# Kernel tuning notes

Hardware: AMD Instinct MI355X
Metric: run time of the kernel (lower is better)

Reference implementation:

```python
import jax, jax.numpy as jnp
import numpy as np

NEG_BIG = -9e15  # matches torch's -9000000000000000.0 masked-fill value
ALPHA = 0.2      # LeakyReLU negative slope


def setup_inputs() -> dict:
    key = jax.random.key(0)
    k1, k2, k3, k4 = jax.random.split(key, 4)
    N, F_in, F_out = 8192, 128, 64
    h = jax.random.normal(k1, (N, F_in), dtype=jnp.float32)
    adj = jax.random.randint(k2, (N, N), 0, 2).astype(jnp.float32)
    # Glorot(gain=1.414)-scale params
    W = jax.random.normal(k3, (F_in, F_out), dtype=jnp.float32) * (1.414 * np.sqrt(2.0 / (F_in + F_out)))
    a = jax.random.normal(k4, (2 * F_out, 1), dtype=jnp.float32) * (1.414 * np.sqrt(2.0 / (2 * F_out + 1)))
    return {"h": h, "adj": adj, "W": W, "a": a}


def reference(h, adj, W, a):
    F_out = W.shape[1]
    Wh = h @ W                               # [N, F_out]
    Wh1 = Wh @ a[:F_out, :]                  # [N, 1]
    Wh2 = Wh @ a[F_out:, :]                  # [N, 1]
    e = jax.nn.leaky_relu(Wh1 + Wh2.T, negative_slope=ALPHA)  # [N, N]
    attention = jnp.where(adj > 0, e, NEG_BIG)
    attention = jax.nn.softmax(attention, axis=1)
    # dropout omitted (eval mode / p applied only in training)
    h_prime = attention @ Wh                 # [N, F_out]
    return jax.nn.elu(h_prime)               # concat=True -> ELU
```

## Files before the change

kernel.cpp:

```cpp
#include <hip/hip_runtime.h>
#include <hip/hip_bf16.h>

#define N 8192
#define FIN 128
#define FOUT 64
#define ALPHA 0.2f
#define LOG2E 1.44269504f
#define JSPLIT 4
#define JSPAN (N / JSPLIT)
#define STJ 128
#define NST (JSPAN / STJ)

typedef __attribute__((ext_vector_type(8))) short short8;
typedef __attribute__((ext_vector_type(4))) float f32x4;

static __device__ __forceinline__ unsigned fkey(float x) {
    unsigned u = __float_as_uint(x);
    return (u >> 31) ? ~u : (u | 0x80000000u);
}
static __device__ __forceinline__ float fdecode(unsigned k) {
    unsigned u = (k & 0x80000000u) ? (k & 0x7FFFFFFFu) : ~k;
    return __uint_as_float(u);
}
static __device__ __forceinline__ void gll16(const float* g, float* l) {
    __builtin_amdgcn_global_load_lds(
        (const __attribute__((address_space(1))) unsigned int*)g,
        (__attribute__((address_space(3))) unsigned int*)l, 16, 0, 0);
}

__global__ __launch_bounds__(256) void k_prep(const float* __restrict__ h,
                                              const float* __restrict__ W,
                                              const float* __restrict__ a,
                                              float* __restrict__ Wh,
                                              float* __restrict__ s2,
                                              float* __restrict__ t2,
                                              unsigned* __restrict__ keys) {
    __shared__ float lH[16 * FIN];
    __shared__ float lW[FIN * FOUT];
    __shared__ float red[8];
    const int tid = threadIdx.x;
    const int r0 = blockIdx.x * 16;
    {
        const float4* src = (const float4*)(h + (size_t)r0 * FIN);
        float4* dst = (float4*)lH;
        for (int i = tid; i < 16 * FIN / 4; i += 256) dst[i] = src[i];
        const float4* ws_ = (const float4*)W;
        float4* dw = (float4*)lW;
        for (int i = tid; i < FIN * FOUT / 4; i += 256) dw[i] = ws_[i];
    }
    __syncthreads();
    const int wave = tid >> 6, lane = tid & 63;
    float acc[4] = {0.f, 0.f, 0.f, 0.f};
    for (int k = 0; k < FIN; ++k) {
        float wv = lW[k * FOUT + lane];
#pragma unroll
        for (int r = 0; r < 4; ++r)
            acc[r] = fmaf(lH[(wave * 4 + r) * FIN + k], wv, acc[r]);
    }
    const float a1 = a[lane], a2 = a[FOUT + lane];
    float smx = -1e30f, tmx = -1e30f;
#pragma unroll
    for (int r = 0; r < 4; ++r) {
        int row = r0 + wave * 4 + r;
        Wh[(size_t)row * FOUT + lane] = acc[r];
        float sv = acc[r] * a1, tv = acc[r] * a2;
#pragma unroll
        for (int off = 32; off; off >>= 1) {
            sv += __shfl_xor(sv, off);
            tv += __shfl_xor(tv, off);
        }
        sv *= LOG2E; tv *= LOG2E;
        if (lane == 0) { s2[row] = sv; t2[row] = tv; }
        smx = fmaxf(smx, sv);
        tmx = fmaxf(tmx, tv);
    }
    if (lane == 0) { red[wave] = smx; red[4 + wave] = tmx; }
    __syncthreads();
    if (tid == 0) {
        float ms = fmaxf(fmaxf(red[0], red[1]), fmaxf(red[2], red[3]));
        float mt = fmaxf(fmaxf(red[4], red[5]), fmaxf(red[6], red[7]));
        atomicMax(keys + 0, fkey(ms));
        atomicMax(keys + 1, fkey(mt));
    }
}

__global__ __launch_bounds__(256) void k_pack(const float* __restrict__ Wh,
                                              __hip_bfloat16* __restrict__ WhB) {
    const int c = blockIdx.x;
    const int tn = threadIdx.x >> 6;
    const int lane = threadIdx.x & 63;
    const int quad = lane >> 4, l16 = lane & 15;
    const float* src = Wh + ((size_t)(c * 32 + quad * 8)) * FOUT + tn * 16 + l16;
    union { unsigned short u[8]; short8 v; } frag;
#pragma unroll
    for (int e = 0; e < 8; ++e) {
        __hip_bfloat16 b = __float2bfloat16(src[(size_t)e * FOUT]);
        frag.u[e] = *(unsigned short*)&b;
    }
    *(short8*)&WhB[(((size_t)c * 4 + tn) * 64 + lane) * 8] = frag.v;
}

__global__ __launch_bounds__(256) void k_attn(const float* __restrict__ adj,
                                              const __hip_bfloat16* __restrict__ WhB,
                                              const float* __restrict__ s2,
                                              const float* __restrict__ t2,
                                              const unsigned* __restrict__ keys,
                                              float* __restrict__ acc_ws,
                                              float* __restrict__ l_ws) {
    __shared__ float smem[2 * 4 * 512];
    __shared__ float smT[2][256];
    __shared__ float shl[4][16];
    const int wave = threadIdx.x >> 6, lane = threadIdx.x & 63;
    const int quad = lane >> 4, l16 = lane & 15;
    const int i0 = blockIdx.x * 16;
    const int jbase = blockIdx.y * JSPAN;

    const float mraw = fdecode(keys[0]) + fdecode(keys[1]);
    const float mm = mraw > 0.f ? mraw : ALPHA * mraw;
    const float sm = s2[i0 + l16];
    const short8* BF = (const short8*)WhB;

    const float* ga = adj + (size_t)(i0 + l16) * N + jbase + wave * 32 + quad * 8;
    const float* gt = t2 + jbase + lane * 4;

    f32x4 acc0 = {0,0,0,0}, acc1 = {0,0,0,0}, acc2 = {0,0,0,0}, acc3 = {0,0,0,0};
    float lsum = 0.f;

    gll16(ga, smem + wave * 512);
    gll16(ga + 4, smem + wave * 512 + 256);
    if (wave == 0) gll16(gt, smT[0]);
    __syncthreads();

    for (int st = 0; st < NST; ++st) {
        const int b = st & 1;
        if (st + 1 < NST) {
            const float* g = ga + (size_t)(st + 1) * STJ;
            float* lb = smem + (b ^ 1) * 2048 + wave * 512;
            gll16(g, lb);
            gll16(g + 4, lb + 256);
            if (wave == 0) gll16(gt + (size_t)(st + 1) * STJ, smT[b ^ 1]);
        }
        const int kc = blockIdx.y * (JSPAN / 32) + st * 4 + wave;
        short8 Bf0 = BF[((size_t)kc * 4 + 0) * 64 + lane];
        short8 Bf1 = BF[((size_t)kc * 4 + 1) * 64 + lane];
        short8 Bf2 = BF[((size_t)kc * 4 + 2) * 64 + lane];
        short8 Bf3 = BF[((size_t)kc * 4 + 3) * 64 + lane];
        const float* Au = smem + b * 2048 + wave * 512;
        float4 alo = *(const float4*)(Au + (lane << 2));
        float4 ahi = *(const float4*)(Au + 256 + (lane << 2));
        const float* Tu = smT[b] + wave * 32 + quad * 8;
        float4 tlo = *(const float4*)(Tu);
        float4 thi = *(const float4*)(Tu + 4);

        union { __hip_bfloat162 h2[4]; short8 v; } af;
#pragma unroll
        for (int pp = 0; pp < 4; ++pp) {
            float a0 = (pp < 2) ? ((const float*)&alo)[2 * pp]     : ((const float*)&ahi)[2 * pp - 4];
            float a1 = (pp < 2) ? ((const float*)&alo)[2 * pp + 1] : ((const float*)&ahi)[2 * pp - 3];
            float t0 = (pp < 2) ? ((const float*)&tlo)[2 * pp]     : ((const float*)&thi)[2 * pp - 4];
            float t1 = (pp < 2) ? ((const float*)&tlo)[2 * pp + 1] : ((const float*)&thi)[2 * pp - 3];
            float x0 = sm + t0,            x1 = sm + t1;
            float le0 = fmaxf(x0, ALPHA * x0), le1 = fmaxf(x1, ALPHA * x1);
            float p0 = a0 * exp2f(le0 - mm),   p1 = a1 * exp2f(le1 - mm);
            __hip_bfloat162 pb = __float22bfloat162_rn(make_float2(p0, p1));
            af.h2[pp] = pb;
            lsum += __bfloat162float(pb.x) + __bfloat162float(pb.y);
        }
        acc0 = __builtin_amdgcn_mfma_f32_16x16x32_bf16(af.v, Bf0, acc0, 0, 0, 0);
        acc1 = __builtin_amdgcn_mfma_f32_16x16x32_bf16(af.v, Bf1, acc1, 0, 0, 0);
        acc2 = __builtin_amdgcn_mfma_f32_16x16x32_bf16(af.v, Bf2, acc2, 0, 0, 0);
        acc3 = __builtin_amdgcn_mfma_f32_16x16x32_bf16(af.v, Bf3, acc3, 0, 0, 0);
        __syncthreads();
    }

    lsum += __shfl_xor(lsum, 16);
    lsum += __shfl_xor(lsum, 32);

    float* accr = smem;
    *(f32x4*)&accr[((wave * 4 + 0) * 64 + lane) * 4] = acc0;
    *(f32x4*)&accr[((wave * 4 + 1) * 64 + lane) * 4] = acc1;
    *(f32x4*)&accr[((wave * 4 + 2) * 64 + lane) * 4] = acc2;
    *(f32x4*)&accr[((wave * 4 + 3) * 64 + lane) * 4] = acc3;
    if (lane < 16) shl[wave][lane] = lsum;
    __syncthreads();

    const int tile = wave;
    f32x4 tot = {0, 0, 0, 0};
#pragma unroll
    for (int w = 0; w < 4; ++w) {
        f32x4 c = *(const f32x4*)&accr[((w * 4 + tile) * 64 + lane) * 4];
        tot[0] += c[0]; tot[1] += c[1]; tot[2] += c[2]; tot[3] += c[3];
    }
#pragma unroll
    for (int r = 0; r < 4; ++r) {
        int row = quad * 4 + r;
        atomicAdd(&acc_ws[(size_t)(i0 + row) * FOUT + tile * 16 + l16], tot[r]);
    }
    if (wave == 0 && lane < 16) {
        float lv = shl[0][lane] + shl[1][lane] + shl[2][lane] + shl[3][lane];
        atomicAdd(&l_ws[i0 + lane], lv);
    }
}

__global__ __launch_bounds__(256) void k_final(const float* __restrict__ acc_ws,
                                               const float* __restrict__ l_ws,
                                               float* __restrict__ out) {
    const int idx = blockIdx.x * 256 + threadIdx.x;
    const int row = idx >> 4;
    const float inv = 1.0f / l_ws[row];
    float4 a = ((const float4*)acc_ws)[idx];
    float4 o;
#pragma unroll
    for (int r = 0; r < 4; ++r) {
        float v = ((const float*)&a)[r] * inv;
        ((float*)&o)[r] = v > 0.f ? v : (exp2f(v * LOG2E) - 1.f);
    }
    ((float4*)out)[idx] = o;
}

extern "C" void kernel_launch(void* const* d_in, const int* in_sizes, int n_in,
                              void* d_out, int out_size, void* d_ws, size_t ws_size,
                              hipStream_t stream) {
    const float* h   = (const float*)d_in[0];
    const float* adj = (const float*)d_in[1];
    const float* W   = (const float*)d_in[2];
    const float* a   = (const float*)d_in[3];
    float* out = (float*)d_out;

    float* Wh = (float*)d_ws;
    __hip_bfloat16* WhB = (__hip_bfloat16*)(Wh + (size_t)N * FOUT);
    float* s2 = (float*)(WhB + (size_t)N * FOUT);
    float* t2 = s2 + N;
    float* pad = t2 + N;
    float* acc_ws = pad + 256;
    float* l_ws = acc_ws + (size_t)N * FOUT;
    unsigned* keys = (unsigned*)(l_ws + N);

    hipMemsetAsync(acc_ws, 0, ((size_t)N * FOUT + N) * sizeof(float) + 2 * sizeof(unsigned),
                   stream);
    k_prep<<<N / 16, 256, 0, stream>>>(h, W, a, Wh, s2, t2, keys);
    k_pack<<<N / 32, 256, 0, stream>>>(Wh, WhB);
    dim3 ag(N / 16, JSPLIT);
    k_attn<<<ag, 256, 0, stream>>>(adj, WhB, s2, t2, keys, acc_ws, l_ws);
    k_final<<<(N * FOUT / 4) / 256, 256, 0, stream>>>(acc_ws, l_ws, out);
}
```

Measured before the change: 415.7 us.

## Split attention into streaming P-matrix kernel and separate MFMA PV kernel

Replaces the fused adjacency-to-MFMA kernel with two passes. The first pass streams adj, computes the masked exp weights, writes them as a bf16 matrix and accumulates row sums. The second pass does a register-prefetched MFMA product into per-split partial buffers, which the final kernel reduces instead of relying on atomics. This trades extra global traffic and a large workspace for simpler, more bandwidth-friendly kernels without LDS sync in the main loop.

```diff
diff --git a/kernel.cpp b/kernel.cpp
--- a/kernel.cpp
+++ b/kernel.cpp
@@ -6,10 +6,9 @@
 #define FOUT 64
 #define ALPHA 0.2f
 #define LOG2E 1.44269504f
-#define JSPLIT 4
-#define JSPAN (N / JSPLIT)
-#define STJ 128
-#define NST (JSPAN / STJ)
+#define KSPLIT 8
+#define KSPAN (N / KSPLIT)
+#define UPW 8
 
 typedef __attribute__((ext_vector_type(8))) short short8;
 typedef __attribute__((ext_vector_type(4))) float f32x4;
@@ -21,11 +20,6 @@
 static __device__ __forceinline__ float fdecode(unsigned k) {
     unsigned u = (k & 0x80000000u) ? (k & 0x7FFFFFFFu) : ~k;
     return __uint_as_float(u);
-}
-static __device__ __forceinline__ void gll16(const float* g, float* l) {
-    __builtin_amdgcn_global_load_lds(
-        (const __attribute__((address_space(1))) unsigned int*)g,
-        (__attribute__((address_space(3))) unsigned int*)l, 16, 0, 0);
 }
 
 __global__ __launch_bounds__(256) void k_prep(const float* __restrict__ h,
@@ -100,105 +94,94 @@
     *(short8*)&WhB[(((size_t)c * 4 + tn) * 64 + lane) * 8] = frag.v;
 }
 
-__global__ __launch_bounds__(256) void k_attn(const float* __restrict__ adj,
-                                              const __hip_bfloat16* __restrict__ WhB,
+__global__ __launch_bounds__(256) void k_pmat(const float* __restrict__ adj,
                                               const float* __restrict__ s2,
                                               const float* __restrict__ t2,
                                               const unsigned* __restrict__ keys,
-                                              float* __restrict__ acc_ws,
+                                              unsigned long long* __restrict__ P,
                                               float* __restrict__ l_ws) {
-    __shared__ float smem[2 * 4 * 512];
-    __shared__ float smT[2][256];
-    __shared__ float shl[4][16];
+    const int tid = blockIdx.x * 256 + threadIdx.x;
+    const int row = tid >> 11;
+    const int j4 = tid & 2047;
+    const int lane = threadIdx.x & 63;
+    const float mraw = fdecode(keys[0]) + fdecode(keys[1]);
+    const float mm = mraw > 0.f ? mraw : ALPHA * mraw;
+    const float sm = s2[row];
+    const float4 av = ((const float4*)adj)[tid];
+    const float4 tv = ((const float4*)t2)[j4];
+    float p[4];
+#pragma unroll
+    for (int e = 0; e < 4; ++e) {
+        float x = sm + ((const float*)&tv)[e];
+        float le = fmaxf(x, ALPHA * x);
+        p[e] = ((const float*)&av)[e] * exp2f(le - mm);
+    }
+    union { __hip_bfloat162 h2[2]; unsigned long long u64; } pk;
+    pk.h2[0] = __float22bfloat162_rn(make_float2(p[0], p[1]));
+    pk.h2[1] = __float22bfloat162_rn(make_float2(p[2], p[3]));
+    P[tid] = pk.u64;
+    float ls = __bfloat162float(pk.h2[0].x) + __bfloat162float(pk.h2[0].y) +
+               __bfloat162float(pk.h2[1].x) + __bfloat162float(pk.h2[1].y);
+#pragma unroll
+    for (int off = 32; off; off >>= 1) ls += __shfl_xor(ls, off);
+    if (lane == 0) atomicAdd(&l_ws[row], ls);
+}
+
+__global__ __launch_bounds__(256) void k_pv(const __hip_bfloat16* __restrict__ P,
+                                            const __hip_bfloat16* __restrict__ WhB,
+                                            float* __restrict__ acc_ws) {
+    __shared__ float ep[4][4][64][4];
     const int wave = threadIdx.x >> 6, lane = threadIdx.x & 63;
     const int quad = lane >> 4, l16 = lane & 15;
     const int i0 = blockIdx.x * 16;
-    const int jbase = blockIdx.y * JSPAN;
-
-    const float mraw = fdecode(keys[0]) + fdecode(keys[1]);
-    const float mm = mraw > 0.f ? mraw : ALPHA * mraw;
-    const float sm = s2[i0 + l16];
+    const int kb = blockIdx.y * KSPAN + wave * 256;
+    const int kc0 = blockIdx.y * (KSPAN / 32) + wave * UPW;
+    const short8* PG = (const short8*)(P + (size_t)(i0 + l16) * N + kb + quad * 8);
     const short8* BF = (const short8*)WhB;
 
-    const float* ga = adj + (size_t)(i0 + l16) * N + jbase + wave * 32 + quad * 8;
-    const float* gt = t2 + jbase + lane * 4;
-
     f32x4 acc0 = {0,0,0,0}, acc1 = {0,0,0,0}, acc2 = {0,0,0,0}, acc3 = {0,0,0,0};
-    float lsum = 0.f;
-
-    gll16(ga, smem + wave * 512);
-    gll16(ga + 4, smem + wave * 512 + 256);
-    if (wave == 0) gll16(gt, smT[0]);
+    short8 Pp[2], B0[2], B1[2], B2[2], B3[2];
+#pragma unroll
+    for (int d = 0; d < 2; ++d) {
+        Pp[d] = PG[d * 4];
+        const size_t c = (size_t)(kc0 + d) * 4;
+        B0[d] = BF[(c + 0) * 64 + lane];
+        B1[d] = BF[(c + 1) * 64 + lane];
+        B2[d] = BF[(c + 2) * 64 + lane];
+        B3[d] = BF[(c + 3) * 64 + lane];
+    }
+#pragma unroll
+    for (int u = 0; u < UPW; ++u) {
+        const int sl = u & 1;
+        acc0 = __builtin_amdgcn_mfma_f32_16x16x32_bf16(Pp[sl], B0[sl], acc0, 0, 0, 0);
+        acc1 = __builtin_amdgcn_mfma_f32_16x16x32_bf16(Pp[sl], B1[sl], acc1, 0, 0, 0);
+        acc2 = __builtin_amdgcn_mfma_f32_16x16x32_bf16(Pp[sl], B2[sl], acc2, 0, 0, 0);
+        acc3 = __builtin_amdgcn_mfma_f32_16x16x32_bf16(Pp[sl], B3[sl], acc3, 0, 0, 0);
+        int un = u + 2; if (un > UPW - 1) un = UPW - 1;
+        Pp[sl] = PG[un * 4];
+        const size_t c = (size_t)(kc0 + un) * 4;
+        B0[sl] = BF[(c + 0) * 64 + lane];
+        B1[sl] = BF[(c + 1) * 64 + lane];
+        B2[sl] = BF[(c + 2) * 64 + lane];
+        B3[sl] = BF[(c + 3) * 64 + lane];
+    }
+
+    *(f32x4*)&ep[wave][0][lane][0] = acc0;
+    *(f32x4*)&ep[wave][1][lane][0] = acc1;
+    *(f32x4*)&ep[wave][2][lane][0] = acc2;
+    *(f32x4*)&ep[wave][3][lane][0] = acc3;
     __syncthreads();
-
-    for (int st = 0; st < NST; ++st) {
-        const int b = st & 1;
-        if (st + 1 < NST) {
-            const float* g = ga + (size_t)(st + 1) * STJ;
-            float* lb = smem + (b ^ 1) * 2048 + wave * 512;
-            gll16(g, lb);
-            gll16(g + 4, lb + 256);
-            if (wave == 0) gll16(gt + (size_t)(st + 1) * STJ, smT[b ^ 1]);
-        }
-        const int kc = blockIdx.y * (JSPAN / 32) + st * 4 + wave;
-        short8 Bf0 = BF[((size_t)kc * 4 + 0) * 64 + lane];
-        short8 Bf1 = BF[((size_t)kc * 4 + 1) * 64 + lane];
-        short8 Bf2 = BF[((size_t)kc * 4 + 2) * 64 + lane];
-        short8 Bf3 = BF[((size_t)kc * 4 + 3) * 64 + lane];
-        const float* Au = smem + b * 2048 + wave * 512;
-        float4 alo = *(const float4*)(Au + (lane << 2));
-        float4 ahi = *(const float4*)(Au + 256 + (lane << 2));
-        const float* Tu = smT[b] + wave * 32 + quad * 8;
-        float4 tlo = *(const float4*)(Tu);
-        float4 thi = *(const float4*)(Tu + 4);
-
-        union { __hip_bfloat162 h2[4]; short8 v; } af;
-#pragma unroll
-        for (int pp = 0; pp < 4; ++pp) {
-            float a0 = (pp < 2) ? ((const float*)&alo)[2 * pp]     : ((const float*)&ahi)[2 * pp - 4];
-            float a1 = (pp < 2) ? ((const float*)&alo)[2 * pp + 1] : ((const float*)&ahi)[2 * pp - 3];
-            float t0 = (pp < 2) ? ((const float*)&tlo)[2 * pp]     : ((const float*)&thi)[2 * pp - 4];
-            float t1 = (pp < 2) ? ((const float*)&tlo)[2 * pp + 1] : ((const float*)&thi)[2 * pp - 3];
-            float x0 = sm + t0,            x1 = sm + t1;
-            float le0 = fmaxf(x0, ALPHA * x0), le1 = fmaxf(x1, ALPHA * x1);
-            float p0 = a0 * exp2f(le0 - mm),   p1 = a1 * exp2f(le1 - mm);
-            __hip_bfloat162 pb = __float22bfloat162_rn(make_float2(p0, p1));
-            af.h2[pp] = pb;
-            lsum += __bfloat162float(pb.x) + __bfloat162float(pb.y);
-        }
-        acc0 = __builtin_amdgcn_mfma_f32_16x16x32_bf16(af.v, Bf0, acc0, 0, 0, 0);
-        acc1 = __builtin_amdgcn_mfma_f32_16x16x32_bf16(af.v, Bf1, acc1, 0, 0, 0);
-        acc2 = __builtin_amdgcn_mfma_f32_16x16x32_bf16(af.v, Bf2, acc2, 0, 0, 0);
-        acc3 = __builtin_amdgcn_mfma_f32_16x16x32_bf16(af.v, Bf3, acc3, 0, 0, 0);
-        __syncthreads();
-    }
-
-    lsum += __shfl_xor(lsum, 16);
-    lsum += __shfl_xor(lsum, 32);
-
-    float* accr = smem;
-    *(f32x4*)&accr[((wave * 4 + 0) * 64 + lane) * 4] = acc0;
-    *(f32x4*)&accr[((wave * 4 + 1) * 64 + lane) * 4] = acc1;
-    *(f32x4*)&accr[((wave * 4 + 2) * 64 + lane) * 4] = acc2;
-    *(f32x4*)&accr[((wave * 4 + 3) * 64 + lane) * 4] = acc3;
-    if (lane < 16) shl[wave][lane] = lsum;
-    __syncthreads();
-
-    const int tile = wave;
     f32x4 tot = {0, 0, 0, 0};
 #pragma unroll
     for (int w = 0; w < 4; ++w) {
-        f32x4 c = *(const f32x4*)&accr[((w * 4 + tile) * 64 + lane) * 4];
+        f32x4 c = *(const f32x4*)&ep[w][wave][lane][0];
         tot[0] += c[0]; tot[1] += c[1]; tot[2] += c[2]; tot[3] += c[3];
     }
+    float* dst = acc_ws + ((size_t)blockIdx.y * N + i0) * FOUT;
 #pragma unroll
     for (int r = 0; r < 4; ++r) {
         int row = quad * 4 + r;
-        atomicAdd(&acc_ws[(size_t)(i0 + row) * FOUT + tile * 16 + l16], tot[r]);
-    }
-    if (wave == 0 && lane < 16) {
-        float lv = shl[0][lane] + shl[1][lane] + shl[2][lane] + shl[3][lane];
-        atomicAdd(&l_ws[i0 + lane], lv);
+        dst[(size_t)row * FOUT + wave * 16 + l16] = tot[r];
     }
 }
 
@@ -208,11 +191,16 @@
     const int idx = blockIdx.x * 256 + threadIdx.x;
     const int row = idx >> 4;
     const float inv = 1.0f / l_ws[row];
-    float4 a = ((const float4*)acc_ws)[idx];
+    float4 sum = {0.f, 0.f, 0.f, 0.f};
+#pragma unroll
+    for (int ks = 0; ks < KSPLIT; ++ks) {
+        float4 a = ((const float4*)(acc_ws + (size_t)ks * N * FOUT))[idx];
+        sum.x += a.x; sum.y += a.y; sum.z += a.z; sum.w += a.w;
+    }
     float4 o;
 #pragma unroll
     for (int r = 0; r < 4; ++r) {
-        float v = ((const float*)&a)[r] * inv;
+        float v = ((const float*)&sum)[r] * inv;
         ((float*)&o)[r] = v > 0.f ? v : (exp2f(v * LOG2E) - 1.f);
     }
     ((float4*)out)[idx] = o;
@@ -227,20 +215,21 @@
     const float* a   = (const float*)d_in[3];
     float* out = (float*)d_out;
 
-    float* Wh = (float*)d_ws;
-    __hip_bfloat16* WhB = (__hip_bfloat16*)(Wh + (size_t)N * FOUT);
-    float* s2 = (float*)(WhB + (size_t)N * FOUT);
-    float* t2 = s2 + N;
-    float* pad = t2 + N;
-    float* acc_ws = pad + 256;
-    float* l_ws = acc_ws + (size_t)N * FOUT;
-    unsigned* keys = (unsigned*)(l_ws + N);
-
-    hipMemsetAsync(acc_ws, 0, ((size_t)N * FOUT + N) * sizeof(float) + 2 * sizeof(unsigned),
-                   stream);
+    char* base = (char*)d_ws;
+    float* Wh = (float*)base;                               base += (size_t)N * FOUT * 4;
+    __hip_bfloat16* WhB = (__hip_bfloat16*)base;            base += (size_t)N * FOUT * 2;
+    float* s2 = (float*)base;                               base += (size_t)N * 4;
+    float* t2 = (float*)base;                               base += (size_t)N * 4;
+    float* l_ws = (float*)base;                             base += (size_t)N * 4;
+    unsigned* keys = (unsigned*)base;                       base += 1024;
+    unsigned long long* P = (unsigned long long*)base;      base += (size_t)N * N * 2;
+    float* acc_ws = (float*)base;
+
+    hipMemsetAsync(l_ws, 0, (size_t)N * 4 + 1024, stream);
     k_prep<<<N / 16, 256, 0, stream>>>(h, W, a, Wh, s2, t2, keys);
     k_pack<<<N / 32, 256, 0, stream>>>(Wh, WhB);
-    dim3 ag(N / 16, JSPLIT);
-    k_attn<<<ag, 256, 0, stream>>>(adj, WhB, s2, t2, keys, acc_ws, l_ws);
-    k_final<<<(N * FOUT / 4) / 256, 256, 0, stream>>>(acc_ws, l_ws, out);
-}
+    k_pmat<<<(size_t)N * N / 4 / 256, 256, 0, stream>>>(adj, s2, t2, keys, P, l_ws);
+    dim3 pvg(N / 16, KSPLIT);
+    k_pv<<<pvg, 256, 0, stream>>>((const __hip_bfloat16*)P, WhB, acc_ws);
+    k_final<<<N * FOUT / 4 / 256, 256, 0, stream>>>(acc_ws, l_ws, out);
+}
```

New measurement: 473.6 us. +13.9%, slower.

## Double stage width and preload t2 span into LDS in attention kernel

Applied to the files above, without the earlier changes.

Each pipeline stage now covers 256 columns, with every wave handling two 32-column chunks, which halves the number of block barriers per j-span. The whole t2 slice for the block's span is copied into LDS once up front instead of being streamed per stage. The B fragment loads are hoisted above the async adj prefetch and fenced with sched_barrier to control instruction ordering. LDS use grows to about 40 KB per block, which may lower occupancy, and each wave holds more registers for eight B fragments.

```diff
diff --git a/kernel.cpp b/kernel.cpp
--- a/kernel.cpp
+++ b/kernel.cpp
@@ -8,7 +8,7 @@
 #define LOG2E 1.44269504f
 #define JSPLIT 4
 #define JSPAN (N / JSPLIT)
-#define STJ 128
+#define STJ 256
 #define NST (JSPAN / STJ)
 
 typedef __attribute__((ext_vector_type(8))) short short8;
@@ -107,81 +107,103 @@
                                               const unsigned* __restrict__ keys,
                                               float* __restrict__ acc_ws,
                                               float* __restrict__ l_ws) {
-    __shared__ float smem[2 * 4 * 512];
-    __shared__ float smT[2][256];
-    __shared__ float shl[4][16];
+    __shared__ float bufA[2][8 * 512];
+    __shared__ float tl[JSPAN];
     const int wave = threadIdx.x >> 6, lane = threadIdx.x & 63;
     const int quad = lane >> 4, l16 = lane & 15;
     const int i0 = blockIdx.x * 16;
-    const int jbase = blockIdx.y * JSPAN;
+    const int jb = blockIdx.y * JSPAN;
+    const int u0 = 2 * wave;
+
+    {
+        const float4* src = (const float4*)(t2 + jb);
+        float4* dst = (float4*)tl;
+        for (int i = threadIdx.x; i < JSPAN / 4; i += 256) dst[i] = src[i];
+    }
+    const float* gaw = adj + (size_t)(i0 + l16) * N + jb + quad * 8;
+    gll16(gaw + u0 * 32,      &bufA[0][u0 * 512]);
+    gll16(gaw + u0 * 32 + 4,  &bufA[0][u0 * 512 + 256]);
+    gll16(gaw + u0 * 32 + 32, &bufA[0][(u0 + 1) * 512]);
+    gll16(gaw + u0 * 32 + 36, &bufA[0][(u0 + 1) * 512 + 256]);
 
     const float mraw = fdecode(keys[0]) + fdecode(keys[1]);
     const float mm = mraw > 0.f ? mraw : ALPHA * mraw;
     const float sm = s2[i0 + l16];
     const short8* BF = (const short8*)WhB;
 
-    const float* ga = adj + (size_t)(i0 + l16) * N + jbase + wave * 32 + quad * 8;
-    const float* gt = t2 + jbase + lane * 4;
-
     f32x4 acc0 = {0,0,0,0}, acc1 = {0,0,0,0}, acc2 = {0,0,0,0}, acc3 = {0,0,0,0};
     float lsum = 0.f;
-
-    gll16(ga, smem + wave * 512);
-    gll16(ga + 4, smem + wave * 512 + 256);
-    if (wave == 0) gll16(gt, smT[0]);
     __syncthreads();
 
     for (int st = 0; st < NST; ++st) {
         const int b = st & 1;
+        const size_t kc = (size_t)(blockIdx.y * (JSPAN / 32) + st * 8 + u0) * 4;
+        short8 B00 = BF[(kc + 0) * 64 + lane];
+        short8 B01 = BF[(kc + 1) * 64 + lane];
+        short8 B02 = BF[(kc + 2) * 64 + lane];
+        short8 B03 = BF[(kc + 3) * 64 + lane];
+        short8 B10 = BF[(kc + 4) * 64 + lane];
+        short8 B11 = BF[(kc + 5) * 64 + lane];
+        short8 B12 = BF[(kc + 6) * 64 + lane];
+        short8 B13 = BF[(kc + 7) * 64 + lane];
+        __builtin_amdgcn_sched_barrier(0);
         if (st + 1 < NST) {
-            const float* g = ga + (size_t)(st + 1) * STJ;
-            float* lb = smem + (b ^ 1) * 2048 + wave * 512;
-            gll16(g, lb);
-            gll16(g + 4, lb + 256);
-            if (wave == 0) gll16(gt + (size_t)(st + 1) * STJ, smT[b ^ 1]);
+            const float* g = gaw + (st + 1) * STJ + u0 * 32;
+            float* d = &bufA[b ^ 1][u0 * 512];
+            gll16(g, d);
+            gll16(g + 4, d + 256);
+            gll16(g + 32, d + 512);
+            gll16(g + 36, d + 768);
         }
-        const int kc = blockIdx.y * (JSPAN / 32) + st * 4 + wave;
-        short8 Bf0 = BF[((size_t)kc * 4 + 0) * 64 + lane];
-        short8 Bf1 = BF[((size_t)kc * 4 + 1) * 64 + lane];
-        short8 Bf2 = BF[((size_t)kc * 4 + 2) * 64 + lane];
-        short8 Bf3 = BF[((size_t)kc * 4 + 3) * 64 + lane];
-        const float* Au = smem + b * 2048 + wave * 512;
-        float4 alo = *(const float4*)(Au + (lane << 2));
-        float4 ahi = *(const float4*)(Au + 256 + (lane << 2));
-        const float* Tu = smT[b] + wave * 32 + quad * 8;
-        float4 tlo = *(const float4*)(Tu);
-        float4 thi = *(const float4*)(Tu + 4);
-
-        union { __hip_bfloat162 h2[4]; short8 v; } af;
-#pragma unroll
-        for (int pp = 0; pp < 4; ++pp) {
-            float a0 = (pp < 2) ? ((const float*)&alo)[2 * pp]     : ((const float*)&ahi)[2 * pp - 4];
-            float a1 = (pp < 2) ? ((const float*)&alo)[2 * pp + 1] : ((const float*)&ahi)[2 * pp - 3];
-            float t0 = (pp < 2) ? ((const float*)&tlo)[2 * pp]     : ((const float*)&thi)[2 * pp - 4];
-            float t1 = (pp < 2) ? ((const float*)&tlo)[2 * pp + 1] : ((const float*)&thi)[2 * pp - 3];
-            float x0 = sm + t0,            x1 = sm + t1;
-            float le0 = fmaxf(x0, ALPHA * x0), le1 = fmaxf(x1, ALPHA * x1);
-            float p0 = a0 * exp2f(le0 - mm),   p1 = a1 * exp2f(le1 - mm);
-            __hip_bfloat162 pb = __float22bfloat162_rn(make_float2(p0, p1));
-            af.h2[pp] = pb;
-            lsum += __bfloat162float(pb.x) + __bfloat162float(pb.y);
+        __builtin_amdgcn_sched_barrier(0);
+#pragma unroll
+        for (int uu = 0; uu < 2; ++uu) {
+            const int ul = u0 + uu;
+            const float* Au = &bufA[b][ul * 512];
+            float4 alo = *(const float4*)(Au + lane * 4);
+            float4 ahi = *(const float4*)(Au + 256 + lane * 4);
+            const float* Tp = tl + st * STJ + ul * 32 + quad * 8;
+            float4 tlo = *(const float4*)Tp;
+            float4 thi = *(const float4*)(Tp + 4);
+            union { __hip_bfloat162 h2[4]; short8 v; } af;
+#pragma unroll
+            for (int pp = 0; pp < 4; ++pp) {
+                float a0 = (pp < 2) ? ((const float*)&alo)[2 * pp]     : ((const float*)&ahi)[2 * pp - 4];
+                float a1 = (pp < 2) ? ((const float*)&alo)[2 * pp + 1] : ((const float*)&ahi)[2 * pp - 3];
+                float t0 = (pp < 2) ? ((const float*)&tlo)[2 * pp]     : ((const float*)&thi)[2 * pp - 4];
+                float t1 = (pp < 2) ? ((const float*)&tlo)[2 * pp + 1] : ((const float*)&thi)[2 * pp - 3];
+                float x0 = sm + t0,                x1 = sm + t1;
+                float le0 = fmaxf(x0, ALPHA * x0), le1 = fmaxf(x1, ALPHA * x1);
+                float p0 = a0 * exp2f(le0 - mm),   p1 = a1 * exp2f(le1 - mm);
+                __hip_bfloat162 pb = __float22bfloat162_rn(make_float2(p0, p1));
+                af.h2[pp] = pb;
+                lsum += __bfloat162float(pb.x) + __bfloat162float(pb.y);
+            }
+            if (uu == 0) {
+                acc0 = __builtin_amdgcn_mfma_f32_16x16x32_bf16(af.v, B00, acc0, 0, 0, 0);
+                acc1 = __builtin_amdgcn_mfma_f32_16x16x32_bf16(af.v, B01, acc1, 0, 0, 0);
+                acc2 = __builtin_amdgcn_mfma_f32_16x16x32_bf16(af.v, B02, acc2, 0, 0, 0);
+                acc3 = __builtin_amdgcn_mfma_f32_16x16x32_bf16(af.v, B03, acc3, 0, 0, 0);
+            } else {
+                acc0 = __builtin_amdgcn_mfma_f32_16x16x32_bf16(af.v, B10, acc0, 0, 0, 0);
+                acc1 = __builtin_amdgcn_mfma_f32_16x16x32_bf16(af.v, B11, acc1, 0, 0, 0);
+                acc2 = __builtin_amdgcn_mfma_f32_16x16x32_bf16(af.v, B12, acc2, 0, 0, 0);
+                acc3 = __builtin_amdgcn_mfma_f32_16x16x32_bf16(af.v, B13, acc3, 0, 0, 0);
+            }
         }
-        acc0 = __builtin_amdgcn_mfma_f32_16x16x32_bf16(af.v, Bf0, acc0, 0, 0, 0);
-        acc1 = __builtin_amdgcn_mfma_f32_16x16x32_bf16(af.v, Bf1, acc1, 0, 0, 0);
-        acc2 = __builtin_amdgcn_mfma_f32_16x16x32_bf16(af.v, Bf2, acc2, 0, 0, 0);
-        acc3 = __builtin_amdgcn_mfma_f32_16x16x32_bf16(af.v, Bf3, acc3, 0, 0, 0);
         __syncthreads();
     }
 
     lsum += __shfl_xor(lsum, 16);
     lsum += __shfl_xor(lsum, 32);
 
-    float* accr = smem;
+    float* accr = &bufA[0][0];
+    float* shlp = tl;
     *(f32x4*)&accr[((wave * 4 + 0) * 64 + lane) * 4] = acc0;
     *(f32x4*)&accr[((wave * 4 + 1) * 64 + lane) * 4] = acc1;
     *(f32x4*)&accr[((wave * 4 + 2) * 64 + lane) * 4] = acc2;
     *(f32x4*)&accr[((wave * 4 + 3) * 64 + lane) * 4] = acc3;
-    if (lane < 16) shl[wave][lane] = lsum;
+    if (lane < 16) shlp[wave * 16 + lane] = lsum;
     __syncthreads();
 
     const int tile = wave;
@@ -197,7 +219,7 @@
         atomicAdd(&acc_ws[(size_t)(i0 + row) * FOUT + tile * 16 + l16], tot[r]);
     }
     if (wave == 0 && lane < 16) {
-        float lv = shl[0][lane] + shl[1][lane] + shl[2][lane] + shl[3][lane];
+        float lv = shlp[lane] + shlp[16 + lane] + shlp[32 + lane] + shlp[48 + lane];
         atomicAdd(&l_ws[i0 + lane], lv);
     }
 }
@@ -227,20 +249,19 @@
     const float* a   = (const float*)d_in[3];
     float* out = (float*)d_out;
 
-    float* Wh = (float*)d_ws;
-    __hip_bfloat16* WhB = (__hip_bfloat16*)(Wh + (size_t)N * FOUT);
-    float* s2 = (float*)(WhB + (size_t)N * FOUT);
-    float* t2 = s2 + N;
-    float* pad = t2 + N;
-    float* acc_ws = pad + 256;
-    float* l_ws = acc_ws + (size_t)N * FOUT;
-    unsigned* keys = (unsigned*)(l_ws + N);
-
-    hipMemsetAsync(acc_ws, 0, ((size_t)N * FOUT + N) * sizeof(float) + 2 * sizeof(unsigned),
-                   stream);
+    char* base = (char*)d_ws;
+    float* Wh = (float*)base;                        base += (size_t)N * FOUT * 4;
+    __hip_bfloat16* WhB = (__hip_bfloat16*)base;     base += (size_t)N * FOUT * 2;
+    float* s2 = (float*)base;                        base += (size_t)N * 4;
+    float* t2 = (float*)base;                        base += (size_t)N * 4 + 1024;
+    float* acc_ws = (float*)base;                    base += (size_t)N * FOUT * 4;
+    float* l_ws = (float*)base;                      base += (size_t)N * 4;
+    unsigned* keys = (unsigned*)base;
+
+    hipMemsetAsync(acc_ws, 0, ((size_t)N * FOUT + N) * 4 + 2 * sizeof(unsigned), stream);
     k_prep<<<N / 16, 256, 0, stream>>>(h, W, a, Wh, s2, t2, keys);
     k_pack<<<N / 32, 256, 0, stream>>>(Wh, WhB);
     dim3 ag(N / 16, JSPLIT);
     k_attn<<<ag, 256, 0, stream>>>(adj, WhB, s2, t2, keys, acc_ws, l_ws);
-    k_final<<<(N * FOUT / 4) / 256, 256, 0, stream>>>(acc_ws, l_ws, out);
-}
+    k_final<<<N * FOUT / 4 / 256, 256, 0, stream>>>(acc_ws, l_ws, out);
+}
```

Result: faster. 399.1 us (-4.0%).

## Replace LDS-staged adj pipeline with per-wave register double-buffering and MFMA row sums

Applied to the files above, without the earlier changes.

The attention kernel no longer stages adj and t2 tiles through shared memory with global_load_lds and a block-wide barrier every step. Each wave now owns a contiguous 512-column slice, loads adj, t2 and the packed Wh fragments straight into registers two units ahead, and runs with no barriers in the main loop. The softmax denominator is computed with an extra MFMA against a ones vector instead of scalar adds plus shuffles. This is meant to cut barrier stalls and LDS traffic on the memory-bound adj stream, at the cost of more registers and a less coalesced per-wave access pattern. The clamped prefetch indices also make the final iteration issue redundant loads.

```diff
diff --git a/kernel.cpp b/kernel.cpp
--- a/kernel.cpp
+++ b/kernel.cpp
@@ -8,8 +8,6 @@
 #define LOG2E 1.44269504f
 #define JSPLIT 4
 #define JSPAN (N / JSPLIT)
-#define STJ 128
-#define NST (JSPAN / STJ)
 
 typedef __attribute__((ext_vector_type(8))) short short8;
 typedef __attribute__((ext_vector_type(4))) float f32x4;
@@ -21,11 +19,6 @@
 static __device__ __forceinline__ float fdecode(unsigned k) {
     unsigned u = (k & 0x80000000u) ? (k & 0x7FFFFFFFu) : ~k;
     return __uint_as_float(u);
-}
-static __device__ __forceinline__ void gll16(const float* g, float* l) {
-    __builtin_amdgcn_global_load_lds(
-        (const __attribute__((address_space(1))) unsigned int*)g,
-        (__attribute__((address_space(3))) unsigned int*)l, 16, 0, 0);
 }
 
 __global__ __launch_bounds__(256) void k_prep(const float* __restrict__ h,
@@ -107,98 +100,103 @@
                                               const unsigned* __restrict__ keys,
                                               float* __restrict__ acc_ws,
                                               float* __restrict__ l_ws) {
-    __shared__ float smem[2 * 4 * 512];
-    __shared__ float smT[2][256];
-    __shared__ float shl[4][16];
+    __shared__ float ep[4][4][64][4];
     const int wave = threadIdx.x >> 6, lane = threadIdx.x & 63;
     const int quad = lane >> 4, l16 = lane & 15;
     const int i0 = blockIdx.x * 16;
-    const int jbase = blockIdx.y * JSPAN;
+    const int jw = blockIdx.y * JSPAN + wave * 512;
+
+    const float* ga = adj + (size_t)(i0 + l16) * N + jw + quad * 8;
+    const float* gt = t2 + jw + quad * 8;
+    const int cb = jw >> 5;
+    const short8* BF = (const short8*)WhB;
 
     const float mraw = fdecode(keys[0]) + fdecode(keys[1]);
     const float mm = mraw > 0.f ? mraw : ALPHA * mraw;
     const float sm = s2[i0 + l16];
-    const short8* BF = (const short8*)WhB;
-
-    const float* ga = adj + (size_t)(i0 + l16) * N + jbase + wave * 32 + quad * 8;
-    const float* gt = t2 + jbase + lane * 4;
+
+    const short8 onesv = {0x3F80, 0x3F80, 0x3F80, 0x3F80, 0x3F80, 0x3F80, 0x3F80, 0x3F80};
 
     f32x4 acc0 = {0,0,0,0}, acc1 = {0,0,0,0}, acc2 = {0,0,0,0}, acc3 = {0,0,0,0};
-    float lsum = 0.f;
-
-    gll16(ga, smem + wave * 512);
-    gll16(ga + 4, smem + wave * 512 + 256);
-    if (wave == 0) gll16(gt, smT[0]);
+    f32x4 accL = {0,0,0,0};
+
+    float4 Aa[2], Ab[2], Ta[2], Tb[2];
+    short8 B0[2], B1[2], B2[2], B3[2];
+
+#define LOADU(s, u)                                                              \
+    do {                                                                         \
+        Aa[s] = *(const float4*)(ga + (u) * 32);                                 \
+        Ab[s] = *(const float4*)(ga + (u) * 32 + 4);                             \
+        Ta[s] = *(const float4*)(gt + (u) * 32);                                 \
+        Tb[s] = *(const float4*)(gt + (u) * 32 + 4);                             \
+        const size_t c_ = (size_t)(cb + (u)) * 4;                                \
+        B0[s] = BF[(c_ + 0) * 64 + lane];                                        \
+        B1[s] = BF[(c_ + 1) * 64 + lane];                                        \
+        B2[s] = BF[(c_ + 2) * 64 + lane];                                        \
+        B3[s] = BF[(c_ + 3) * 64 + lane];                                        \
+    } while (0)
+
+#define PROCU(s)                                                                 \
+    do {                                                                         \
+        union { __hip_bfloat162 h2[4]; short8 v; } af;                           \
+        _Pragma("unroll")                                                        \
+        for (int pp = 0; pp < 4; ++pp) {                                         \
+            float a0 = (pp < 2) ? ((const float*)&Aa[s])[2 * pp]                 \
+                                : ((const float*)&Ab[s])[2 * pp - 4];            \
+            float a1 = (pp < 2) ? ((const float*)&Aa[s])[2 * pp + 1]             \
+                                : ((const float*)&Ab[s])[2 * pp - 3];            \
+            float t0 = (pp < 2) ? ((const float*)&Ta[s])[2 * pp]                 \
+                                : ((const float*)&Tb[s])[2 * pp - 4];            \
+            float t1 = (pp < 2) ? ((const float*)&Ta[s])[2 * pp + 1]             \
+                                : ((const float*)&Tb[s])[2 * pp - 3];            \
+            float x0 = sm + t0, x1 = sm + t1;                                    \
+            float le0 = fmaxf(x0, ALPHA * x0), le1 = fmaxf(x1, ALPHA * x1);      \
+            float p0 = a0 * exp2f(le0 - mm), p1 = a1 * exp2f(le1 - mm);          \
+            af.h2[pp] = __float22bfloat162_rn(make_float2(p0, p1));              \
+        }                                                                        \
+        acc0 = __builtin_amdgcn_mfma_f32_16x16x32_bf16(af.v, B0[s], acc0, 0, 0, 0); \
+        acc1 = __builtin_amdgcn_mfma_f32_16x16x32_bf16(af.v, B1[s], acc1, 0, 0, 0); \
+        acc2 = __builtin_amdgcn_mfma_f32_16x16x32_bf16(af.v, B2[s], acc2, 0, 0, 0); \
+        acc3 = __builtin_amdgcn_mfma_f32_16x16x32_bf16(af.v, B3[s], acc3, 0, 0, 0); \
+        accL = __builtin_amdgcn_mfma_f32_16x16x32_bf16(af.v, onesv, accL, 0, 0, 0); \
+    } while (0)
+
+    LOADU(0, 0);
+    LOADU(1, 1);
+#pragma unroll 1
+    for (int k = 0; k < 8; ++k) {
+        PROCU(0);
+        PROCU(1);
+        const int u0 = (2 * k + 2 > 14) ? 14 : 2 * k + 2;
+        const int u1 = (2 * k + 3 > 15) ? 15 : 2 * k + 3;
+        LOADU(0, u0);
+        LOADU(1, u1);
+    }
+#undef LOADU
+#undef PROCU
+
+    if (l16 == 0) {
+#pragma unroll
+        for (int r = 0; r < 4; ++r)
+            atomicAdd(&l_ws[i0 + quad * 4 + r], accL[r]);
+    }
+
+    *(f32x4*)&ep[wave][0][lane][0] = acc0;
+    *(f32x4*)&ep[wave][1][lane][0] = acc1;
+    *(f32x4*)&ep[wave][2][lane][0] = acc2;
+    *(f32x4*)&ep[wave][3][lane][0] = acc3;
     __syncthreads();
-
-    for (int st = 0; st < NST; ++st) {
-        const int b = st & 1;
-        if (st + 1 < NST) {
-            const float* g = ga + (size_t)(st + 1) * STJ;
-            float* lb = smem + (b ^ 1) * 2048 + wave * 512;
-            gll16(g, lb);
-            gll16(g + 4, lb + 256);
-            if (wave == 0) gll16(gt + (size_t)(st + 1) * STJ, smT[b ^ 1]);
-        }
-        const int kc = blockIdx.y * (JSPAN / 32) + st * 4 + wave;
-        short8 Bf0 = BF[((size_t)kc * 4 + 0) * 64 + lane];
-        short8 Bf1 = BF[((size_t)kc * 4 + 1) * 64 + lane];
-        short8 Bf2 = BF[((size_t)kc * 4 + 2) * 64 + lane];
-        short8 Bf3 = BF[((size_t)kc * 4 + 3) * 64 + lane];
-        const float* Au = smem + b * 2048 + wave * 512;
-        float4 alo = *(const float4*)(Au + (lane << 2));
-        float4 ahi = *(const float4*)(Au + 256 + (lane << 2));
-        const float* Tu = smT[b] + wave * 32 + quad * 8;
-        float4 tlo = *(const float4*)(Tu);
-        float4 thi = *(const float4*)(Tu + 4);
-
-        union { __hip_bfloat162 h2[4]; short8 v; } af;
-#pragma unroll
-        for (int pp = 0; pp < 4; ++pp) {
-            float a0 = (pp < 2) ? ((const float*)&alo)[2 * pp]     : ((const float*)&ahi)[2 * pp - 4];
-            float a1 = (pp < 2) ? ((const float*)&alo)[2 * pp + 1] : ((const float*)&ahi)[2 * pp - 3];
-            float t0 = (pp < 2) ? ((const float*)&tlo)[2 * pp]     : ((const float*)&thi)[2 * pp - 4];
-            float t1 = (pp < 2) ? ((const float*)&tlo)[2 * pp + 1] : ((const float*)&thi)[2 * pp - 3];
-            float x0 = sm + t0,            x1 = sm + t1;
-            float le0 = fmaxf(x0, ALPHA * x0), le1 = fmaxf(x1, ALPHA * x1);
-            float p0 = a0 * exp2f(le0 - mm),   p1 = a1 * exp2f(le1 - mm);
-            __hip_bfloat162 pb = __float22bfloat162_rn(make_float2(p0, p1));
-            af.h2[pp] = pb;
-            lsum += __bfloat162float(pb.x) + __bfloat162float(pb.y);
-        }
-        acc0 = __builtin_amdgcn_mfma_f32_16x16x32_bf16(af.v, Bf0, acc0, 0, 0, 0);
-        acc1 = __builtin_amdgcn_mfma_f32_16x16x32_bf16(af.v, Bf1, acc1, 0, 0, 0);
-        acc2 = __builtin_amdgcn_mfma_f32_16x16x32_bf16(af.v, Bf2, acc2, 0, 0, 0);
-        acc3 = __builtin_amdgcn_mfma_f32_16x16x32_bf16(af.v, Bf3, acc3, 0, 0, 0);
-        __syncthreads();
-    }
-
-    lsum += __shfl_xor(lsum, 16);
-    lsum += __shfl_xor(lsum, 32);
-
-    float* accr = smem;
-    *(f32x4*)&accr[((wave * 4 + 0) * 64 + lane) * 4] = acc0;
-    *(f32x4*)&accr[((wave * 4 + 1) * 64 + lane) * 4] = acc1;
-    *(f32x4*)&accr[((wave * 4 + 2) * 64 + lane) * 4] = acc2;
-    *(f32x4*)&accr[((wave * 4 + 3) * 64 + lane) * 4] = acc3;
-    if (lane < 16) shl[wave][lane] = lsum;
-    __syncthreads();
-
     const int tile = wave;
     f32x4 tot = {0, 0, 0, 0};
 #pragma unroll
     for (int w = 0; w < 4; ++w) {
-        f32x4 c = *(const f32x4*)&accr[((w * 4 + tile) * 64 + lane) * 4];
+        f32x4 c = *(const f32x4*)&ep[w][tile][lane][0];
         tot[0] += c[0]; tot[1] += c[1]; tot[2] += c[2]; tot[3] += c[3];
     }
 #pragma unroll
     for (int r = 0; r < 4; ++r) {
         int row = quad * 4 + r;
         atomicAdd(&acc_ws[(size_t)(i0 + row) * FOUT + tile * 16 + l16], tot[r]);
-    }
-    if (wave == 0 && lane < 16) {
-        float lv = shl[0][lane] + shl[1][lane] + shl[2][lane] + shl[3][lane];
-        atomicAdd(&l_ws[i0 + lane], lv);
     }
 }
 
@@ -227,20 +225,19 @@
     const float* a   = (const float*)d_in[3];
     float* out = (float*)d_out;
 
-    float* Wh = (float*)d_ws;
-    __hip_bfloat16* WhB = (__hip_bfloat16*)(Wh + (size_t)N * FOUT);
-    float* s2 = (float*)(WhB + (size_t)N * FOUT);
-    float* t2 = s2 + N;
-    float* pad = t2 + N;
-    float* acc_ws = pad + 256;
-    float* l_ws = acc_ws + (size_t)N * FOUT;
-    unsigned* keys = (unsigned*)(l_ws + N);
-
-    hipMemsetAsync(acc_ws, 0, ((size_t)N * FOUT + N) * sizeof(float) + 2 * sizeof(unsigned),
-                   stream);
+    char* base = (char*)d_ws;
+    float* Wh = (float*)base;                        base += (size_t)N * FOUT * 4;
+    __hip_bfloat16* WhB = (__hip_bfloat16*)base;     base += (size_t)N * FOUT * 2;
+    float* s2 = (float*)base;                        base += (size_t)N * 4;
+    float* t2 = (float*)base;                        base += (size_t)N * 4 + 1024;
+    float* acc_ws = (float*)base;                    base += (size_t)N * FOUT * 4;
+    float* l_ws = (float*)base;                      base += (size_t)N * 4;
+    unsigned* keys = (unsigned*)base;
+
+    hipMemsetAsync(acc_ws, 0, ((size_t)N * FOUT + N) * 4 + 2 * sizeof(unsigned), stream);
     k_prep<<<N / 16, 256, 0, stream>>>(h, W, a, Wh, s2, t2, keys);
     k_pack<<<N / 32, 256, 0, stream>>>(Wh, WhB);
     dim3 ag(N / 16, JSPLIT);
     k_attn<<<ag, 256, 0, stream>>>(adj, WhB, s2, t2, keys, acc_ws, l_ws);
-    k_final<<<(N * FOUT / 4) / 256, 256, 0, stream>>>(acc_ws, l_ws, out);
-}
+    k_final<<<N * FOUT / 4 / 256, 256, 0, stream>>>(acc_ws, l_ws, out);
+}
```

Measured after the change: 428.0 us. 3.0% more time.
